# Performance work log

Measured on AMD Instinct MI355X. Metric: run time of the kernel, lower is better.

Reference implementation:

```python
import jax, jax.numpy as jnp
import numpy as np

# Cubic B-spline prefilter (Unser 1993), periodic ('wrap') boundary.
POLE = float(np.sqrt(3.0) - 2.0)   # single pole of cubic B-spline
GAIN = 6.0                          # (1 - z) * (1 - 1/z) for the cubic pole


def _prefilter_axis(x, axis):
    """Causal + anticausal IIR recursion along `axis`, periodic boundary."""
    z = jnp.asarray(POLE, x.dtype)
    N = x.shape[axis]
    xm = jnp.moveaxis(x, axis, 0)          # (N, ...)
    c = xm * jnp.asarray(GAIN, x.dtype)
    zN = z ** N
    k = jnp.arange(1, N, dtype=x.dtype)
    # causal init (periodic steady state):
    #   c+(0) = (c(0) + sum_{k=1..N-1} z^k c(N-k)) / (1 - z^N)
    c0 = (c[0] + jnp.tensordot(z ** k, c[1:][::-1], axes=(0, 0))) / (1 - zN)

    def fwd(carry, ci):                    # c+(n) = c(n) + z * c+(n-1)
        new = ci + z * carry
        return new, new

    _, cp_rest = jax.lax.scan(fwd, c0, c[1:])
    cp = jnp.concatenate([c0[None], cp_rest], axis=0)

    # anticausal init (periodic steady state):
    #   c-(N-1) = -(z/(1-z^N)) * sum_{k=0..N-1} z^k c+((N-1+k) mod N)
    k2 = jnp.arange(N, dtype=x.dtype)
    cp_rolled = jnp.roll(cp, 1, axis=0)    # cp_rolled[k] = cp[(N-1+k) % N]
    cm_last = -(z / (1 - zN)) * jnp.tensordot(z ** k2, cp_rolled, axes=(0, 0))

    def bwd(carry, cpi):                   # c-(n) = z * (c-(n+1) - c+(n))
        new = z * (carry - cpi)
        return new, new

    _, cm_rev = jax.lax.scan(bwd, cm_last, cp[N - 2::-1])
    cm = jnp.concatenate([cm_rev[::-1], cm_last[None]], axis=0)
    return jnp.moveaxis(cm, 0, axis)


def setup_inputs() -> dict:
    key = jax.random.key(0)
    x = jax.random.normal(key, (2, 3, 160, 160, 160), dtype=jnp.float32)
    return {"x": x}


def reference(x):
    # ToCoeff.forward: filter every spatial axis (dims 2..) with the
    # cubic spline prefilter; channel movedim is a no-op mathematically.
    ndim = x.ndim - 2
    out = x
    for ax in range(2, 2 + ndim):
        out = _prefilter_axis(out, ax)
    return out
```

## Files before the change

### kernel.cpp

```cpp
#include <hip/hip_runtime.h>


#define NAX   160
#define PLN   25600
#define VOL   4096000
#define ZP    (-0.26794919243112270647f)
#define KW    16

__global__ __launch_bounds__(256, 5)
void pass_d2(const float* __restrict__ in, float* __restrict__ out)
{
    const float z = ZP;
    const int l     = threadIdx.x & 63;
    const int chunk = threadIdx.x >> 6;
    const int L = blockIdx.x * 64 + l;
    const int v = L / PLN;
    const int i = L - v * PLN;
    const float* src = in  + (size_t)v * VOL + i;
    float*       dst = out + (size_t)v * VOL + i;
    const int n0 = chunk * 40;

    float st = 0.0f;
    #pragma unroll
    for (int s = 0; s < KW; ++s) {
        int r = n0 - KW + s; if (r < 0) r += NAX;
        st = fmaf(z, st, 6.0f * src[(size_t)r * PLN]);
    }
    float cp[56];
    #pragma unroll
    for (int s = 0; s < 56; ++s) {
        int r = n0 + s; if (r >= NAX) r -= NAX;
        st = fmaf(z, st, 6.0f * src[(size_t)r * PLN]);
        cp[s] = st;
    }
    float sm = 0.0f;
    #pragma unroll
    for (int s = 55; s >= 40; --s) sm = z * (sm - cp[s]);
    #pragma unroll
    for (int s = 39; s >= 0; --s) {
        sm = z * (sm - cp[s]);
        dst[(size_t)(n0 + s) * PLN] = sm;
    }
}

__device__ __forceinline__ int swz(int r, int c) {
    return r * NAX + (c ^ (r & 31));
}

__global__ __launch_bounds__(320, 6)
void slab_d3d4(const float* __restrict__ src, float* __restrict__ dst)
{
    __shared__ float Y[40 * NAX];
    const float z = ZP;
    const int tid = threadIdx.x;

    const int b   = blockIdx.x;
    const int q   = (b >> 3) & 3;
    const int p   = ((b >> 5) << 3) + (b & 7);
    const int R0  = 40 * q;
    const float* pin  = src + (size_t)p * PLN;
    float*       pout = dst + (size_t)p * PLN;

    float f[20];

    {
        const int c  = tid % NAX;
        const int h  = tid / NAX;
        const int n0 = R0 + 20 * h;
        float st = 0.0f;
        #pragma unroll
        for (int s = 0; s < KW; ++s) {
            int r = n0 - KW + s; if (r < 0) r += NAX;
            st = fmaf(z, st, 6.0f * pin[r * NAX + c]);
        }
        #pragma unroll
        for (int s = 0; s < 20; ++s) {
            st = fmaf(z, st, 6.0f * pin[(n0 + s) * NAX + c]);
            f[s] = st;
        }
        float Ta = 0.0f, zp = z;
        #pragma unroll
        for (int k = 0; k < KW; ++k) {
            int r = n0 + 20 + k; if (r >= NAX) r -= NAX;
            st = fmaf(z, st, 6.0f * pin[r * NAX + c]);
            Ta = fmaf(zp, st, Ta);
            zp *= z;
        }
        float sm = -Ta;
        #pragma unroll
        for (int s = 19; s >= 0; --s) { sm = z * (sm - f[s]); f[s] = sm; }

        const int lr0 = 20 * h;
        #pragma unroll
        for (int s = 0; s < 20; ++s)
            Y[swz(lr0 + s, c)] = f[s];
    }
    __syncthreads();

    {
        const int rr = tid >> 3;
        const int mq = tid & 7;
        const int m0 = 20 * mq;
        float st = 0.0f;
        #pragma unroll
        for (int s = 0; s < KW; ++s) {
            int cc = m0 - KW + s; if (cc < 0) cc += NAX;
            st = fmaf(z, st, 6.0f * Y[swz(rr, cc)]);
        }
        #pragma unroll
        for (int s = 0; s < 20; ++s) {
            st = fmaf(z, st, 6.0f * Y[swz(rr, m0 + s)]);
            f[s] = st;
        }
        float Ta = 0.0f, zp = z;
        #pragma unroll
        for (int k = 0; k < KW; ++k) {
            int cc = m0 + 20 + k; if (cc >= NAX) cc -= NAX;
            st = fmaf(z, st, 6.0f * Y[swz(rr, cc)]);
            Ta = fmaf(zp, st, Ta);
            zp *= z;
        }
        float sm = -Ta;
        #pragma unroll
        for (int s = 19; s >= 0; --s) { sm = z * (sm - f[s]); f[s] = sm; }

        __syncthreads();
        #pragma unroll
        for (int s = 0; s < 20; ++s)
            Y[swz(rr, m0 + s)] = f[s];
    }
    __syncthreads();

    #pragma unroll
    for (int k = 0; k < 20; ++k) {
        const int idx = tid + 320 * k;
        const int lr  = idx / NAX;
        const int c   = idx - lr * NAX;
        __builtin_nontemporal_store(Y[swz(lr, c)], &pout[(R0 + lr) * NAX + c]);
    }
}

__global__ __launch_bounds__(640, 2)
void pass_d3d4(float* __restrict__ buf)
{
    __shared__ float P[PLN];
    const float z = ZP;
    const int tid = threadIdx.x;
    float* plane = buf + (size_t)blockIdx.x * PLN;

    const int c  = tid % NAX;
    const int tq = tid / NAX;
    const int n0 = tq * 40;

    #pragma unroll
    for (int k = 0; k < 40; ++k) {
        const int r = 4 * k + tq;
        P[swz(r, c)] = plane[r * NAX + c];
    }
    __syncthreads();

    float f[40];
    {
        float st = 0.0f;
        #pragma unroll
        for (int s = 0; s < KW; ++s) {
            int r = n0 - KW + s; if (r < 0) r += NAX;
            st = fmaf(z, st, 6.0f * P[swz(r, c)]);
        }
        #pragma unroll
        for (int s = 0; s < 40; ++s) {
            st = fmaf(z, st, 6.0f * P[swz(n0 + s, c)]);
            f[s] = st;
        }
        __syncthreads();
        #pragma unroll
        for (int s = 0; s < 40; ++s) P[swz(n0 + s, c)] = f[s];
        __syncthreads();
        float sm = 0.0f;
        #pragma unroll
        for (int s = KW - 1; s >= 0; --s) {
            int r = n0 + 40 + s; if (r >= NAX) r -= NAX;
            sm = z * (sm - P[swz(r, c)]);
        }
        __syncthreads();
        #pragma unroll
        for (int s = 39; s >= 0; --s) { sm = z * (sm - f[s]); P[swz(n0 + s, c)] = sm; }
        __syncthreads();
    }
    {
        const int rr = c;
        float st = 0.0f;
        #pragma unroll
        for (int s = 0; s < KW; ++s) {
            int cc = n0 - KW + s; if (cc < 0) cc += NAX;
            st = fmaf(z, st, 6.0f * P[swz(rr, cc)]);
        }
        #pragma unroll
        for (int s = 0; s < 40; ++s) {
            st = fmaf(z, st, 6.0f * P[swz(rr, n0 + s)]);
            f[s] = st;
        }
        __syncthreads();
        #pragma unroll
        for (int s = 0; s < 40; ++s) P[swz(rr, n0 + s)] = f[s];
        __syncthreads();
        float sm = 0.0f;
        #pragma unroll
        for (int s = KW - 1; s >= 0; --s) {
            int cc = n0 + 40 + s; if (cc >= NAX) cc -= NAX;
            sm = z * (sm - P[swz(rr, cc)]);
        }
        __syncthreads();
        #pragma unroll
        for (int s = 39; s >= 0; --s) { sm = z * (sm - f[s]); P[swz(rr, n0 + s)] = sm; }
        __syncthreads();
    }
    #pragma unroll
    for (int k = 0; k < 40; ++k) {
        const int r = 4 * k + tq;
        plane[r * NAX + c] = P[swz(r, c)];
    }
}

extern "C" void kernel_launch(void* const* d_in, const int* in_sizes, int n_in,
                              void* d_out, int out_size, void* d_ws, size_t ws_size,
                              hipStream_t stream) {
    (void)in_sizes; (void)n_in; (void)out_size;
    const float* x = (const float*)d_in[0];
    float* out = (float*)d_out;
    float* ws  = (float*)d_ws;

    const size_t need = (size_t)6 * VOL * sizeof(float);
    if (ws_size >= need) {
        pass_d2  <<<2400, 256, 0, stream>>>(x, ws);
        slab_d3d4<<<3840, 320, 0, stream>>>(ws, out);
    } else {
        pass_d2  <<<2400, 256, 0, stream>>>(x, out);
        pass_d3d4<<<960,  640, 0, stream>>>(out);
    }
}
```

Baseline: 78.58 us.

## Stage depth-axis columns in shared memory and split the recursion into more chunks

The first-axis pass now loads a 160x64 column tile into shared memory once per block, then runs the windowed IIR recursion from LDS. Eight chunks of 20 samples per column replace the earlier four chunks of 40. Before, each thread read 56+16 global values, re-reading overlapping halos from global memory. Now each global element is read once, at the cost of a 40KB LDS tile per block and a block-wide barrier. The anticausal tail is computed as a weighted sum, matching the slab kernel.

```diff
diff --git a/kernel.cpp b/kernel.cpp
--- a/kernel.cpp
+++ b/kernel.cpp
@@ -7,39 +7,52 @@
 #define ZP    (-0.26794919243112270647f)
 #define KW    16
 
-__global__ __launch_bounds__(256, 5)
-void pass_d2(const float* __restrict__ in, float* __restrict__ out)
+__global__ __launch_bounds__(512, 6)
+void k_d2s(const float* __restrict__ in, float* __restrict__ out)
 {
+    __shared__ float T[NAX * 64];
     const float z = ZP;
-    const int l     = threadIdx.x & 63;
-    const int chunk = threadIdx.x >> 6;
-    const int L = blockIdx.x * 64 + l;
-    const int v = L / PLN;
-    const int i = L - v * PLN;
-    const float* src = in  + (size_t)v * VOL + i;
-    float*       dst = out + (size_t)v * VOL + i;
-    const int n0 = chunk * 40;
-
-    float st = 0.0f;
+    const int t    = threadIdx.x;
+    const int lane = t & 63, wv = t >> 6;
+    const int g  = blockIdx.x;
+    const int v  = g / 400;
+    const int i0 = (g - v * 400) * 64;
+    const float* src = in  + (size_t)v * VOL + i0;
+    float*       dst = out + (size_t)v * VOL + i0;
+
+    #pragma unroll
+    for (int k = 0; k < 20; ++k) {
+        const int r = wv + 8 * k;
+        T[r * 64 + lane] = src[(size_t)r * PLN + lane];
+    }
+    __syncthreads();
+
+    const int c = lane, n0 = wv * 20;
+    float st = 0.f;
     #pragma unroll
     for (int s = 0; s < KW; ++s) {
         int r = n0 - KW + s; if (r < 0) r += NAX;
-        st = fmaf(z, st, 6.0f * src[(size_t)r * PLN]);
-    }
-    float cp[56];
-    #pragma unroll
-    for (int s = 0; s < 56; ++s) {
-        int r = n0 + s; if (r >= NAX) r -= NAX;
-        st = fmaf(z, st, 6.0f * src[(size_t)r * PLN]);
-        cp[s] = st;
-    }
-    float sm = 0.0f;
-    #pragma unroll
-    for (int s = 55; s >= 40; --s) sm = z * (sm - cp[s]);
-    #pragma unroll
-    for (int s = 39; s >= 0; --s) {
-        sm = z * (sm - cp[s]);
-        dst[(size_t)(n0 + s) * PLN] = sm;
+        st = fmaf(z, st, 6.0f * T[r * 64 + c]);
+    }
+    float f[20];
+    #pragma unroll
+    for (int s = 0; s < 20; ++s) {
+        st = fmaf(z, st, 6.0f * T[(n0 + s) * 64 + c]);
+        f[s] = st;
+    }
+    float Ta = 0.f, zp = z;
+    #pragma unroll
+    for (int k = 0; k < KW; ++k) {
+        int r = n0 + 20 + k; if (r >= NAX) r -= NAX;
+        st = fmaf(z, st, 6.0f * T[r * 64 + c]);
+        Ta = fmaf(zp, st, Ta);
+        zp *= z;
+    }
+    float sm = -Ta;
+    #pragma unroll
+    for (int s = 19; s >= 0; --s) {
+        sm = z * (sm - f[s]);
+        dst[(size_t)(n0 + s) * PLN + c] = sm;
     }
 }
 
@@ -232,10 +245,10 @@
 
     const size_t need = (size_t)6 * VOL * sizeof(float);
     if (ws_size >= need) {
-        pass_d2  <<<2400, 256, 0, stream>>>(x, ws);
+        k_d2s    <<<2400, 512, 0, stream>>>(x, ws);
         slab_d3d4<<<3840, 320, 0, stream>>>(ws, out);
     } else {
-        pass_d2  <<<2400, 256, 0, stream>>>(x, out);
+        k_d2s    <<<2400, 512, 0, stream>>>(x, out);
         pass_d3d4<<<960,  640, 0, stream>>>(out);
     }
 }
```

After: 70.81 us. 9.9% less time.
